# Kernel tuning notes

Measured on AMD Instinct MI355X. Metric: run time of the kernel, lower is better.

## Reference

```python
import jax, jax.numpy as jnp
import numpy as np


def topk_activation(x, k):
    # x: [B, L]; keep top-k per row, zeros elsewhere (torch.topk + scatter_)
    vals, idx = jax.lax.top_k(x, k)            # [B, k]
    rows = jnp.arange(x.shape[0])[:, None]     # [B, 1]
    return jnp.zeros_like(x).at[rows, idx].set(vals)


def setup_inputs() -> dict:
    key = jax.random.key(0)
    k0, k1, k2, k3 = jax.random.split(key, 4)
    B, n_in, n_lat = 4096, 768, 24576
    x = jax.random.normal(k0, (B, n_in), dtype=jnp.float32)
    b = jnp.zeros((n_in,), jnp.float32)
    W_enc = jax.random.normal(k1, (n_lat, n_in), dtype=jnp.float32) * 0.02
    b_enc = jnp.zeros((n_lat,), jnp.float32)
    W_dec = jax.random.normal(k2, (n_in, n_lat), dtype=jnp.float32) * 0.02
    # unit L2 norm per decoder column (as in _normalize_decoder)
    W_dec = W_dec / jnp.clip(jnp.linalg.norm(W_dec, axis=0, keepdims=True), 1e-8)
    miss_counts = jax.random.randint(k3, (n_lat,), 0, 2)  # ~half 'dead' (>=1)
    return {"x": x, "b": b, "W_enc": W_enc, "b_enc": b_enc, "W_dec": W_dec,
            "miss_counts": miss_counts, "k": 32, "aux_k": 512}


def reference(x, b, W_enc, b_enc, W_dec, miss_counts, k, aux_k):
    x_centered = x - b                                   # [B, n_in]
    alpha_pre = x_centered @ W_enc.T + b_enc             # [B, n_lat]
    alpha = topk_activation(alpha_pre, k)                # sparse code
    x_hat = alpha @ W_dec.T + b                          # dense decode
    fired_mask = alpha != 0
    # aux dead-feature path; dead_mask = miss_counts >= threshold(=1).
    # With the chosen miss_counts fill, dead count >> aux_k, so
    # min(aux_k, dead.sum()) == aux_k (static for jit).
    dead_mask = miss_counts >= 1                         # [n_lat]
    alpha_pre_dead = jnp.where(dead_mask[None, :], alpha_pre, -jnp.inf)
    alpha_aux = topk_activation(alpha_pre_dead, aux_k)
    aux_x_hat = alpha_aux @ W_dec.T + b
    return x_hat, alpha, fired_mask, aux_x_hat
```

## Files before the change

kernel.cpp:

```cpp
#include <hip/hip_runtime.h>
#include <math.h>

#define NB   4096
#define NIN  768
#define NLAT 24576
#define K2   1536
#define KT2  24

#define BM 128
#define BN 128
#define BK 16
#define LDT 132

#define CAND_CAP 512
#define BAND_CAP 160
#define MAIN_CAP 64
#define AUX_CAP  1024
#define SELT     1024
#define GRP      6

#define CM_CAP 768
#define CA_CAP 2560
#define BB_CAP 384
#define BPSTRIDE (BAND_CAP + 4)

#define OFF_K16  0
#define OFF_REDF 49152
#define OFF_CTRL 49664
#define OFF_PCNT 49792
#define OFF_CKM  50176
#define OFF_CIM  52224
#define OFF_CKA  54272
#define OFF_CIA  56320
#define OFF_BIM  58368
#define OFF_BIA  59008
#define OFF_BVM  59648
#define OFF_BVA  60928
#define OFF_BSM  62208
#define OFF_BSA  62368
#define OFF_REDI 62528
#define SMEM_SEL 62592

typedef __bf16 bf16x8 __attribute__((ext_vector_type(8)));
typedef float  f32x4  __attribute__((ext_vector_type(4)));

__device__ __forceinline__ unsigned fkey(float f) {
  unsigned u = __float_as_uint(f);
  return u ^ ((unsigned)((int)u >> 31) | 0x80000000u);
}
__device__ __forceinline__ float keyinv(unsigned u) {
  unsigned s = (u & 0x80000000u) ? (u ^ 0x80000000u) : ~u;
  return __uint_as_float(s);
}
__device__ __forceinline__ float zup(float p) {
  p = fminf(fmaxf(p, 1e-7f), 0.5f);
  float t = sqrtf(-2.0f * logf(p));
  return t - (2.30753f + 0.27061f * t) / (1.0f + 0.99229f * t + 0.04481f * t * t);
}

#define GLOAD16(g, l) __builtin_amdgcn_global_load_lds( \
    (const __attribute__((address_space(1))) unsigned int*)(g), \
    (__attribute__((address_space(3))) unsigned int*)(l), 16, 0, 0)

__global__ __launch_bounds__(256) void k_deadbits(const int* __restrict__ miss,
                                                  unsigned* __restrict__ bits) {
  int j = blockIdx.x * 256 + threadIdx.x;
  unsigned long long b = __ballot(miss[j] >= 1);
  if ((threadIdx.x & 63) == 0) {
    int w = j >> 5;
    bits[w] = (unsigned)b;
    bits[w + 1] = (unsigned)(b >> 32);
  }
}

__global__ __launch_bounds__(256) void k_ndead(const unsigned* __restrict__ bits,
                                               int* __restrict__ out) {
  __shared__ int w[4];
  int t = threadIdx.x;
  int c = 0;
  for (int i = t; i < NLAT / 32; i += 256) c += __popc(bits[i]);
#pragma unroll
  for (int o = 32; o; o >>= 1) c += __shfl_xor(c, o);
  if ((t & 63) == 0) w[t >> 6] = c;
  __syncthreads();
  if (t == 0) out[0] = w[0] + w[1] + w[2] + w[3];
}

__global__ __launch_bounds__(256) void k_transpose(const float* __restrict__ src,
                                                   __bf16* __restrict__ dst) {
  __shared__ float tile[32][33];
  int bx = blockIdx.x * 32;
  int by = blockIdx.y * 32;
  int tx = threadIdx.x, ty = threadIdx.y;
  for (int i = ty; i < 32; i += 8)
    tile[i][tx] = src[(size_t)(by + i) * NLAT + bx + tx];
  __syncthreads();
  for (int i = ty; i < 32; i += 8)
    dst[(size_t)(bx + i) * NIN + by + tx] = (__bf16)tile[tx][i];
}

__global__ __launch_bounds__(256) void k_pack_a(const float* __restrict__ x,
    const float* __restrict__ bvec, __bf16* __restrict__ A2) {
  const int mt = blockIdx.x, kt = blockIdx.y, t = threadIdx.x;
  __bf16* out = A2 + (((size_t)mt * KT2 + kt) << 13);
#pragma unroll
  for (int i = 0; i < 32; ++i) {
    int idx = i * 256 + t;
    int r = idx >> 6, c2 = idx & 63;
    int kk = c2 ^ ((r & 7) << 3);
    int kg = kt * 64 + kk;
    int k = kg >= 768 ? kg - 768 : kg;
    bool lo = (kg >= 768);
    float v = x[(size_t)(mt * 128 + r) * NIN + k] - bvec[k];
    __bf16 h = (__bf16)v;
    out[idx] = lo ? (__bf16)(v - (float)h) : h;
  }
}

__global__ __launch_bounds__(256) void k_pack_b(const float* __restrict__ We,
    __bf16* __restrict__ B2) {
  const int nt = blockIdx.x, kt = blockIdx.y, t = threadIdx.x;
  __bf16* out = B2 + (((size_t)nt * KT2 + kt) << 13);
#pragma unroll
  for (int i = 0; i < 32; ++i) {
    int idx = i * 256 + t;
    int r = idx >> 6, c2 = idx & 63;
    int kk = c2 ^ ((r & 7) << 3);
    int kg = kt * 64 + kk;
    int k = kg >= 768 ? kg - 768 : kg;
    float v = We[(size_t)(nt * 128 + r) * NIN + k];
    out[idx] = (__bf16)v;
  }
}

__global__ __launch_bounds__(256) void k_gemm_bf16(
    const __bf16* __restrict__ A2, const __bf16* __restrict__ B2,
    const float* __restrict__ be, float* __restrict__ apre) {
  __shared__ char sA[16384];
  __shared__ char sB[16384];
  const int t = threadIdx.x;
  const int lane = t & 63, wave = t >> 6;
  const int mt = blockIdx.x, nt = blockIdx.y;
  const int wm = wave >> 1, wn = wave & 1;

  int aoff[4][2], boff[4][2];
#pragma unroll
  for (int f = 0; f < 4; ++f) {
    int ra = wm * 64 + f * 16 + (lane & 15);
    int rb = wn * 64 + f * 16 + (lane & 15);
#pragma unroll
    for (int kk = 0; kk < 2; ++kk) {
      int c = kk * 64 + (lane >> 4) * 16;
      aoff[f][kk] = ra * 128 + (c ^ ((ra & 7) << 4));
      boff[f][kk] = rb * 128 + (c ^ ((rb & 7) << 4));
    }
  }
  f32x4 acc[4][4] = {};
  const char* gA = (const char*)(A2 + (((size_t)mt * KT2) << 13));
  const char* gB = (const char*)(B2 + (((size_t)nt * KT2) << 13));
  for (int kt = 0; kt < KT2; ++kt) {
    const char* tA = gA + ((size_t)kt << 14);
    const char* tB = gB + ((size_t)kt << 14);
#pragma unroll
    for (int i = 0; i < 4; ++i) {
      int chunk = (i * 4 + wave) * 1024;
      GLOAD16(tA + chunk + lane * 16, sA + chunk);
      GLOAD16(tB + chunk + lane * 16, sB + chunk);
    }
    __syncthreads();
#pragma unroll
    for (int kk = 0; kk < 2; ++kk) {
      bf16x8 a[4], b[4];
#pragma unroll
      for (int f = 0; f < 4; ++f) {
        a[f] = *(const bf16x8*)(sA + aoff[f][kk]);
        b[f] = *(const bf16x8*)(sB + boff[f][kk]);
      }
#pragma unroll
      for (int mi = 0; mi < 4; ++mi)
#pragma unroll
        for (int ni = 0; ni < 4; ++ni)
          acc[mi][ni] = __builtin_amdgcn_mfma_f32_16x16x32_bf16(a[mi], b[ni], acc[mi][ni], 0, 0, 0);
    }
    __syncthreads();
  }
  const int m0 = mt * 128 + wm * 64, n0 = nt * 128 + wn * 64;
#pragma unroll
  for (int ni = 0; ni < 4; ++ni) {
    int n = n0 + ni * 16 + (lane & 15);
    float bb = be[n];
#pragma unroll
    for (int mi = 0; mi < 4; ++mi) {
      int mbase = m0 + mi * 16 + (lane >> 4) * 4;
#pragma unroll
      for (int q = 0; q < 4; ++q)
        apre[(size_t)(mbase + q) * NLAT + n] = acc[mi][ni][q] + bb;
    }
  }
}

__global__ __launch_bounds__(256) void k_encgemm_f32(
    const float* __restrict__ x, const float* __restrict__ bvec,
    const float* __restrict__ We, const float* __restrict__ be,
    float* __restrict__ apre) {
  __shared__ float As[BK][LDT];
  __shared__ float Bs[BK][LDT];
  const int t = threadIdx.x;
  const int m0 = blockIdx.x * BM;
  const int n0 = blockIdx.y * BN;
  const int lane = t & 63, wave = t >> 6;
  const int cn = ((wave & 1) * 8 + (lane & 7)) * 8;
  const int cm = ((wave >> 1) * 8 + (lane >> 3)) * 8;
  float acc[8][8] = {};
  const float* xb = x + (size_t)m0 * NIN;
  const float* wb = We + (size_t)n0 * NIN;
  for (int k0 = 0; k0 < NIN; k0 += BK) {
#pragma unroll
    for (int i = 0; i < 2; ++i) {
      int e = t + i * 256;
      int row = e >> 2, q = e & 3;
      float4 bv = *(const float4*)(bvec + k0 + q * 4);
      float4 av = *(const float4*)(xb + (size_t)row * NIN + k0 + q * 4);
      av.x -= bv.x; av.y -= bv.y; av.z -= bv.z; av.w -= bv.w;
      As[q * 4 + 0][row] = av.x; As[q * 4 + 1][row] = av.y;
      As[q * 4 + 2][row] = av.z; As[q * 4 + 3][row] = av.w;
      float4 wv = *(const float4*)(wb + (size_t)row * NIN + k0 + q * 4);
      Bs[q * 4 + 0][row] = wv.x; Bs[q * 4 + 1][row] = wv.y;
      Bs[q * 4 + 2][row] = wv.z; Bs[q * 4 + 3][row] = wv.w;
    }
    __syncthreads();
#pragma unroll
    for (int kk = 0; kk < BK; ++kk) {
      float a0[8], b0[8];
      *(float4*)&a0[0] = *(const float4*)&As[kk][cm];
      *(float4*)&a0[4] = *(const float4*)&As[kk][cm + 4];
      *(float4*)&b0[0] = *(const float4*)&Bs[kk][cn];
      *(float4*)&b0[4] = *(const float4*)&Bs[kk][cn + 4];
#pragma unroll
      for (int i = 0; i < 8; ++i)
#pragma unroll
        for (int j = 0; j < 8; ++j)
          acc[i][j] = fmaf(a0[i], b0[j], acc[i][j]);
    }
    __syncthreads();
  }
  float bb[8];
  *(float4*)&bb[0] = *(const float4*)(be + n0 + cn);
  *(float4*)&bb[4] = *(const float4*)(be + n0 + cn + 4);
#pragma unroll
  for (int i = 0; i < 8; ++i) {
    float4 v0 = make_float4(acc[i][0] + bb[0], acc[i][1] + bb[1],
                            acc[i][2] + bb[2], acc[i][3] + bb[3]);
    float4 v1 = make_float4(acc[i][4] + bb[4], acc[i][5] + bb[5],
                            acc[i][6] + bb[6], acc[i][7] + bb[7]);
    float* orow = apre + (size_t)(m0 + cm + i) * NLAT + n0 + cn;
    *(float4*)orow = v0;
    *(float4*)(orow + 4) = v1;
  }
}

__global__ __launch_bounds__(1024) void k_select14(
    const float* __restrict__ apre, const float* __restrict__ x,
    const float* __restrict__ bvec, const float* __restrict__ We,
    const float* __restrict__ be, const unsigned* __restrict__ dbits,
    const int* __restrict__ kptr, const int* __restrict__ akptr,
    const int* __restrict__ ndeadP,
    int* __restrict__ cnts, int* __restrict__ mIdxG, float* __restrict__ mValG,
    int* __restrict__ aIdxG, float* __restrict__ aValG,
    int* __restrict__ bandP, int* __restrict__ flags) {
  __shared__ float redF[32];
  __shared__ float statF[4];
  __shared__ int ctrl[24];
  __shared__ int histM[256];
  __shared__ int histA[256];
  __shared__ uint2 cM[CM_CAP];
  __shared__ uint2 cA[CA_CAP];
  __shared__ uint2 bbM[BB_CAP];
  __shared__ uint2 bbA[BB_CAP];
  __shared__ int biM[BAND_CAP];
  __shared__ int biA[BAND_CAP];
  __shared__ double bvM[BAND_CAP];
  __shared__ double bvA[BAND_CAP];
  __shared__ unsigned char bsM[BAND_CAP];
  __shared__ unsigned char bsA[BAND_CAP];
  unsigned* uctrl = (unsigned*)ctrl;

  const int t = threadIdx.x;
  const int r = blockIdx.x;
  const int lane = t & 63, wave = t >> 6;

  if (t < 24) ctrl[t] = 0;
  if (t >= 256 && t < 512) histM[t - 256] = 0;
  else if (t >= 512 && t < 768) histA[t - 512] = 0;

  const uint4* rowp = (const uint4*)(apre + (size_t)r * NLAT);
  unsigned dm = 0;
  float s1 = 0.f, s2 = 0.f;
#pragma unroll
  for (int i = 0; i < GRP; ++i) {
    int g = t + SELT * i;
    uint4 rv = rowp[g];
    unsigned nb = (dbits[g >> 3] >> ((g & 7) * 4)) & 0xFu;
    dm |= nb << (4 * i);
    float vs[4] = {__uint_as_float(rv.x), __uint_as_float(rv.y),
                   __uint_as_float(rv.z), __uint_as_float(rv.w)};
#pragma unroll
    for (int q = 0; q < 4; ++q) { float v = vs[q]; s1 += v; s2 += v * v; }
  }
#pragma unroll
  for (int o = 32; o; o >>= 1) { s1 += __shfl_xor(s1, o); s2 += __shfl_xor(s2, o); }
  if (lane == 0) { redF[wave] = s1; redF[16 + wave] = s2; }
  __syncthreads();
  if (wave == 0) {
    float a0 = (lane < 16) ? redF[lane] : 0.f;
    float a1 = (lane < 16) ? redF[16 + lane] : 0.f;
#pragma unroll
    for (int o = 32; o; o >>= 1) { a0 += __shfl_xor(a0, o); a1 += __shfl_xor(a1, o); }
    if (lane == 0) {
      float mu = a0 / (float)NLAT;
      float var = fmaxf(a1 / (float)NLAT - mu * mu, 1e-20f);
      statF[0] = mu; statF[1] = sqrtf(var);
    }
  }
  __syncthreads();

  int kmain = kptr[0]; if (kmain > MAIN_CAP) kmain = MAIN_CAP;
  int kaux  = akptr[0]; if (kaux > AUX_CAP)  kaux  = AUX_CAP;
  const int ndead = ndeadP[0];
  int kauxE = kaux > ndead ? ndead : kaux;
  const bool mainOn = (kmain > 0);
  const bool auxOn  = (kauxE > 0);
  const float mu = statF[0], sg = statF[1];
  unsigned TkM = 0xFFFFFFFFu, TkA = 0xFFFFFFFFu;
  if (mainOn) TkM = fkey(mu + sg * zup(8.f * kmain / (float)NLAT));
  if (auxOn) {
    float facA = (3.f * kauxE > 2048.f) ? 2.f : 3.f;
    TkA = fkey(mu + sg * zup(facA * kauxE / (float)ndead));
  }

  unsigned mxM = 0u, mxA = 0u;
#pragma unroll
  for (int i = 0; i < GRP; ++i) {
    int g = t + SELT * i;
    uint4 rv = rowp[g];
    unsigned nb = (dm >> (4 * i)) & 0xFu;
    float vs[4] = {__uint_as_float(rv.x), __uint_as_float(rv.y),
                   __uint_as_float(rv.z), __uint_as_float(rv.w)};
#pragma unroll
    for (int q = 0; q < 4; ++q) {
      unsigned kk = fkey(vs[q]);
      unsigned j = (unsigned)(4 * g + q);
      if (mainOn && kk >= TkM) {
        mxM = kk > mxM ? kk : mxM;
        int p = atomicAdd(&ctrl[0], 1);
        if (p < CM_CAP) { cM[p].x = kk; cM[p].y = j; }
      }
      if (auxOn && ((nb >> q) & 1u) && kk >= TkA) {
        mxA = kk > mxA ? kk : mxA;
        int p = atomicAdd(&ctrl[1], 1);
        if (p < CA_CAP) { cA[p].x = kk; cA[p].y = j; }
      }
    }
  }
#pragma unroll
  for (int o = 32; o; o >>= 1) {
    unsigned a = __shfl_xor(mxM, o); mxM = a > mxM ? a : mxM;
    unsigned b = __shfl_xor(mxA, o); mxA = b > mxA ? b : mxA;
  }
  if (lane == 0) { atomicMax(&uctrl[10], mxM); atomicMax(&uctrl[11], mxA); }
  __syncthreads();
  int ccM = ctrl[0], ccA = ctrl[1];
  bool ok = (!mainOn || (ccM >= kmain && ccM <= CM_CAP)) &&
            (!auxOn  || (ccA >= kauxE && ccA <= CA_CAP));
  if (!ok) { if (t == 0) flags[r] = 1; return; }
  if (!auxOn) ccA = 0;
  if (!mainOn) ccM = 0;
  unsigned MxM = uctrl[10], MxA = uctrl[11];
  float sclM = 255.0f / fmaxf((float)(MxM - TkM) + 1.0f, 1.0f);
  float sclA = 255.0f / fmaxf((float)(MxA - TkA) + 1.0f, 1.0f);

  for (int c = t; c < ccM; c += 1024) {
    int b = (int)((float)(cM[c].x - TkM) * sclM);
    b = b < 0 ? 0 : (b > 255 ? 255 : b);
    atomicAdd(&histM[b], 1);
  }
  for (int c = t; c < ccA; c += 1024) {
    int b = (int)((float)(cA[c].x - TkA) * sclA);
    b = b < 0 ? 0 : (b > 255 ? 255 : b);
    atomicAdd(&histA[b], 1);
  }
  __syncthreads();
  if (t == 0 && mainOn) {
    int above = 0, b = 0;
    for (int i = 255; i >= 0; --i) {
      if (above + histM[i] >= kmain) { b = i; break; }
      above += histM[i];
    }
    ctrl[12] = b; ctrl[13] = above;
  }
  if (t == 64 && auxOn) {
    int above = 0, b = 0;
    for (int i = 255; i >= 0; --i) {
      if (above + histA[i] >= kauxE) { b = i; break; }
      above += histA[i];
    }
    ctrl[14] = b; ctrl[15] = above;
  }
  __syncthreads();
  int bM = ctrl[12], aboveM = ctrl[13];
  int bA = ctrl[14], aboveA = ctrl[15];
  for (int c = t; c < ccM; c += 1024) {
    int b = (int)((float)(cM[c].x - TkM) * sclM);
    b = b < 0 ? 0 : (b > 255 ? 255 : b);
    if (b == bM) {
      int p = atomicAdd(&ctrl[16], 1);
      if (p < BB_CAP) bbM[p] = cM[c];
    }
  }
  for (int c = t; c < ccA; c += 1024) {
    int b = (int)((float)(cA[c].x - TkA) * sclA);
    b = b < 0 ? 0 : (b > 255 ? 255 : b);
    if (b == bA) {
      int p = atomicAdd(&ctrl[17], 1);
      if (p < BB_CAP) bbA[p] = cA[c];
    }
  }
  __syncthreads();
  int nbM = ctrl[16], nbA = ctrl[17];
  if ((mainOn && nbM > BB_CAP) || (auxOn && nbA > BB_CAP)) {
    if (t == 0) flags[r] = 1;
    return;
  }
  if (t == 0) flags[r] = 0;
  if (!mainOn) nbM = 0;
  if (!auxOn) nbA = 0;
  if (t < nbM) {
    uint2 e = bbM[t];
    int rank = 0;
    for (int qq = 0; qq < nbM; ++qq) {
      uint2 f = bbM[qq];
      rank += (f.x > e.x || (f.x == e.x && (int)f.y < (int)e.y)) ? 1 : 0;
    }
    if (rank == kmain - aboveM - 1) ctrl[2] = (int)e.x;
  }
  if (t >= 512 && t - 512 < nbA) {
    uint2 e = bbA[t - 512];
    int rank = 0;
    for (int qq = 0; qq < nbA; ++qq) {
      uint2 f = bbA[qq];
      rank += (f.x > e.x || (f.x == e.x && (int)f.y < (int)e.y)) ? 1 : 0;
    }
    if (rank == kauxE - aboveA - 1) ctrl[3] = (int)e.x;
  }
  __syncthreads();

  float VsM = keyinv((unsigned)ctrl[2]);
  float epsM = 1e-2f + 2e-3f * fabsf(VsM);
  unsigned KhiBM = mainOn ? fkey(VsM + epsM) : 0xFFFFFFFFu;
  unsigned KloBM = mainOn ? fkey(VsM - epsM) : 0xFFFFFFFFu;
  float VsA = keyinv((unsigned)ctrl[3]);
  float epsA = 1e-2f + 2e-3f * fabsf(VsA);
  unsigned KhiBA = auxOn ? fkey(VsA + epsA) : 0xFFFFFFFFu;
  unsigned KloBA = auxOn ? fkey(VsA - epsA) : 0xFFFFFFFFu;
  for (int c = t; c < ccM; c += 1024) {
    unsigned kk = cM[c].x;
    if (kk > KhiBM) atomicAdd(&ctrl[4], 1);
    else if (kk >= KloBM) {
      int p = atomicAdd(&ctrl[5], 1);
      if (p < BAND_CAP) biM[p] = (int)cM[c].y;
    }
  }
  for (int c = t; c < ccA; c += 1024) {
    unsigned kk = cA[c].x;
    if (kk > KhiBA) atomicAdd(&ctrl[6], 1);
    else if (kk >= KloBA) {
      int p = atomicAdd(&ctrl[7], 1);
      if (p < BAND_CAP) biA[p] = (int)cA[c].y;
    }
  }
  __syncthreads();
  int nAbM = ctrl[4], bcM = ctrl[5] < BAND_CAP ? ctrl[5] : BAND_CAP;
  int nAbA = ctrl[6], bcA = ctrl[7] < BAND_CAP ? ctrl[7] : BAND_CAP;
  if (!mainOn) bcM = 0;
  if (!auxOn) bcA = 0;
  int needBM = kmain - nAbM; if (needBM < 0) needBM = 0; if (needBM > bcM) needBM = bcM;
  int needBA = kauxE - nAbA; if (needBA < 0) needBA = 0; if (needBA > bcA) needBA = bcA;

  {
    const float* xr = x + (size_t)r * NIN;
    float xb[NIN / 64];
#pragma unroll
    for (int jj = 0; jj < NIN / 64; ++jj) {
      int col = lane + 64 * jj;
      xb[jj] = xr[col] - bvec[col];
    }
    int tot = bcM + bcA;
    for (int m = wave; m < tot; m += 16) {
      int j = (m < bcM) ? biM[m] : biA[m - bcM];
      const float* wr = We + (size_t)j * NIN;
      double s = 0.0;
#pragma unroll
      for (int jj = 0; jj < NIN / 64; ++jj)
        s += (double)xb[jj] * (double)wr[lane + 64 * jj];
#pragma unroll
      for (int o = 32; o; o >>= 1) s += __shfl_xor(s, o);
      if (lane == 0) {
        if (m < bcM) bvM[m] = s + (double)be[j];
        else bvA[m - bcM] = s + (double)be[j];
      }
    }
  }
  __syncthreads();
  if (t < bcM) {
    double vi = bvM[t]; int ii = biM[t];
    double tie = fabs(vi) * 4e-8 + 1e-12;
    int rank = 0;
    for (int qq = 0; qq < bcM; ++qq) {
      double d = bvM[qq] - vi;
      rank += ((fabs(d) <= tie) ? (biM[qq] < ii) : (d > 0.0)) ? 1 : 0;
    }
    bsM[t] = (rank < needBM) ? 1 : 0;
  }
  if (t >= 512 && t - 512 < bcA) {
    int tt = t - 512;
    double vi = bvA[tt]; int ii = biA[tt];
    double tie = fabs(vi) * 4e-8 + 1e-12;
    int rank = 0;
    for (int qq = 0; qq < bcA; ++qq) {
      double d = bvA[qq] - vi;
      rank += ((fabs(d) <= tie) ? (biA[qq] < ii) : (d > 0.0)) ? 1 : 0;
    }
    bsA[tt] = (rank < needBA) ? 1 : 0;
  }
  __syncthreads();

  for (int c = t; c < ccM; c += 1024) {
    unsigned kk = cM[c].x; int j = (int)cM[c].y;
    bool sel = kk > KhiBM;
    if (!sel && kk >= KloBM) {
      for (int m2 = 0; m2 < bcM; ++m2)
        if (biM[m2] == j) { sel = bsM[m2] != 0; break; }
    }
    float v = keyinv(kk);
    if (sel && v != 0.0f) {
      int p = atomicAdd(&ctrl[8], 1);
      if (p < MAIN_CAP) { mIdxG[r * MAIN_CAP + p] = j; mValG[r * MAIN_CAP + p] = v; }
    }
  }
  for (int c = t; c < ccA; c += 1024) {
    unsigned kk = cA[c].x; int j = (int)cA[c].y;
    bool sel = kk > KhiBA;
    if (!sel && kk >= KloBA) {
      for (int m2 = 0; m2 < bcA; ++m2)
        if (biA[m2] == j) { sel = bsA[m2] != 0; break; }
    }
    float v = keyinv(kk);
    if (sel && v != 0.0f) {
      int p = atomicAdd(&ctrl[9], 1);
      if (p < AUX_CAP) { aIdxG[r * AUX_CAP + p] = j; aValG[r * AUX_CAP + p] = v; }
    }
  }
  __syncthreads();
  int* bp = bandP + (size_t)r * BPSTRIDE;
  if (t == 0) {
    cnts[2 * r] = ctrl[8] < MAIN_CAP ? ctrl[8] : MAIN_CAP;
    cnts[2 * r + 1] = auxOn ? (ctrl[9] < AUX_CAP ? ctrl[9] : AUX_CAP) : 0;
    bp[0] = (int)KhiBM; bp[1] = (int)KloBM; bp[2] = bcM;
  }
  if (t < bcM) bp[3 + t] = (biM[t] << 1) | (int)bsM[t];
}

__global__ __launch_bounds__(256) void k_emit(
    const float* apre, const int* __restrict__ flags,
    const int* __restrict__ bandP, float* __restrict__ alpha, float* mask) {
  const int bid = blockIdx.x;
  const int r = bid / 3, c = bid % 3;
  if (flags[r]) return;
  __shared__ int hdr[3];
  __shared__ int bent[BAND_CAP];
  const int t = threadIdx.x;
  const int* bp = bandP + (size_t)r * BPSTRIDE;
  if (t < 3) hdr[t] = bp[t];
  __syncthreads();
  int bc = hdr[2];
  if (t < bc) bent[t] = bp[3 + t];
  __syncthreads();
  unsigned KhiB = (unsigned)hdr[0], KloB = (unsigned)hdr[1];
  const float4* src = (const float4*)(apre + (size_t)r * NLAT) + c * 2048;
  float4* adst = (float4*)(alpha + (size_t)r * NLAT) + c * 2048;
  float4* mdst = (float4*)(mask + (size_t)r * NLAT) + c * 2048;
  const int ebase = c * 8192;
#pragma unroll
  for (int i = 0; i < 8; ++i) {
    int g = t + 256 * i;
    float4 v4 = src[g];
    float vs[4] = {v4.x, v4.y, v4.z, v4.w};
    float av[4], mv[4];
#pragma unroll
    for (int q = 0; q < 4; ++q) {
      float v = vs[q];
      unsigned kk = fkey(v);
      int j = ebase + 4 * g + q;
      bool sel = kk > KhiB;
      if (!sel && kk >= KloB) {
        for (int m = 0; m < bc; ++m)
          if ((bent[m] >> 1) == j) { sel = (bent[m] & 1) != 0; break; }
      }
      av[q] = sel ? v : 0.0f;
      mv[q] = (sel && v != 0.0f) ? 1.0f : 0.0f;
    }
    adst[g] = make_float4(av[0], av[1], av[2], av[3]);
    mdst[g] = make_float4(mv[0], mv[1], mv[2], mv[3]);
  }
}

__global__ __launch_bounds__(SELT) void k_selectFB(
    const float* apre, const float* __restrict__ x,
    const float* __restrict__ bvec, const float* __restrict__ We,
    const float* __restrict__ be, const unsigned* __restrict__ dbits,
    const int* __restrict__ kptr, const int* __restrict__ akptr,
    float* __restrict__ alpha, float* mask,
    int* __restrict__ cnts, int* __restrict__ mIdxG, float* __restrict__ mValG,
    int* __restrict__ aIdxG, float* __restrict__ aValG,
    const int* __restrict__ flags) {
  if (flags[blockIdx.x] == 0) return;
  extern __shared__ char smem[];
  uint2*    keys2 = (uint2*)(smem + OFF_K16);
  float*    redF  = (float*)(smem + OFF_REDF);
  int*      redI  = (int*)(smem + OFF_REDI);
  int*      ctrl  = (int*)(smem + OFF_CTRL);
  float*    ctrlF = (float*)(smem + OFF_CTRL);
  int*      pcnt  = (int*)(smem + OFF_PCNT);
  unsigned* ckM   = (unsigned*)(smem + OFF_CKM);
  int*      ciM   = (int*)(smem + OFF_CIM);
  unsigned* ckA   = (unsigned*)(smem + OFF_CKA);
  int*      ciA   = (int*)(smem + OFF_CIA);
  int*      biM   = (int*)(smem + OFF_BIM);
  int*      biA   = (int*)(smem + OFF_BIA);
  double*   bvM   = (double*)(smem + OFF_BVM);
  double*   bvA   = (double*)(smem + OFF_BVA);
  unsigned char* bsM = (unsigned char*)(smem + OFF_BSM);
  unsigned char* bsA = (unsigned char*)(smem + OFF_BSA);

  const int t = threadIdx.x;
  const int r = blockIdx.x;
  const int lane = t & 63, wave = t >> 6;

  if (t < 96) pcnt[t] = 0;
  else if (t < 108) ctrl[t - 96] = 0;

  const uint4* rowp = (const uint4*)(apre + (size_t)r * NLAT);
  const float* rowf = apre + (size_t)r * NLAT;
  unsigned dm = 0;
  float s1 = 0.f, s2 = 0.f;
  float vmxA = -INFINITY, vmnA = INFINITY, vmxD = -INFINITY, vmnD = INFINITY;
#pragma unroll
  for (int i = 0; i < GRP; ++i) {
    int g = t + SELT * i;
    uint4 rv = rowp[g];
    unsigned nb = (dbits[g >> 3] >> ((g & 7) * 4)) & 0xFu;
    dm |= nb << (4 * i);
    float vs[4] = {__uint_as_float(rv.x), __uint_as_float(rv.y),
                   __uint_as_float(rv.z), __uint_as_float(rv.w)};
    unsigned k16[4];
#pragma unroll
    for (int q = 0; q < 4; ++q) {
      float v = vs[q];
      k16[q] = fkey(v) >> 16;
      s1 += v; s2 += v * v;
      vmxA = fmaxf(vmxA, v); vmnA = fminf(vmnA, v);
      if ((nb >> q) & 1u) { vmxD = fmaxf(vmxD, v); vmnD = fminf(vmnD, v); }
    }
    uint2 kp2;
    kp2.x = k16[0] | (k16[1] << 16);
    kp2.y = k16[2] | (k16[3] << 16);
    keys2[g] = kp2;
  }
  int nd = __popc(dm & 0xFFFFFFu);
#pragma unroll
  for (int o = 32; o; o >>= 1) {
    s1 += __shfl_xor(s1, o); s2 += __shfl_xor(s2, o);
    vmxA = fmaxf(vmxA, __shfl_xor(vmxA, o)); vmnA = fminf(vmnA, __shfl_xor(vmnA, o));
    vmxD = fmaxf(vmxD, __shfl_xor(vmxD, o)); vmnD = fminf(vmnD, __shfl_xor(vmnD, o));
    nd += __shfl_xor(nd, o);
  }
  if (lane == 0) {
    float* rf = redF + wave * 8;
    rf[0] = s1; rf[1] = s2; rf[2] = vmxA; rf[3] = vmnA; rf[4] = vmxD; rf[5] = vmnD;
    redI[wave] = nd;
  }
  __syncthreads();
  if (wave == 0) {
    float a0 = 0.f, a1 = 0.f, a2 = -INFINITY, a3 = INFINITY, a4 = -INFINITY, a5 = INFINITY;
    int a6 = 0;
    if (lane < 16) {
      const float* rf = redF + lane * 8;
      a0 = rf[0]; a1 = rf[1]; a2 = rf[2]; a3 = rf[3]; a4 = rf[4]; a5 = rf[5];
      a6 = redI[lane];
    }
#pragma unroll
    for (int o = 32; o; o >>= 1) {
      a0 += __shfl_xor(a0, o); a1 += __shfl_xor(a1, o);
      a2 = fmaxf(a2, __shfl_xor(a2, o)); a3 = fminf(a3, __shfl_xor(a3, o));
      a4 = fmaxf(a4, __shfl_xor(a4, o)); a5 = fminf(a5, __shfl_xor(a5, o));
      a6 += __shfl_xor(a6, o);
    }
    if (lane == 0) {
      float mu = a0 / (float)NLAT;
      float var = fmaxf(a1 / (float)NLAT - mu * mu, 1e-20f);
      ctrlF[16] = mu; ctrlF[17] = sqrtf(var);
      ctrlF[18] = a3; ctrlF[19] = a2;
      ctrlF[20] = a5; ctrlF[21] = a4;
      ctrl[22] = a6;
    }
  }
  __syncthreads();

  int kmain = kptr[0]; if (kmain > MAIN_CAP) kmain = MAIN_CAP;
  int kaux  = akptr[0]; if (kaux > AUX_CAP)  kaux  = AUX_CAP;
  const float mu = ctrlF[16], sg = ctrlF[17];
  const int ndead = ctrl[22];
  int kauxE = kaux > ndead ? ndead : kaux;
  const bool mainOn = (kmain > 0);
  const bool auxOn  = (kauxE > 0);

  unsigned TloM = fkey(ctrlF[18]) >> 16, ThiM = (fkey(ctrlF[19]) >> 16) + 1u;
  int cLoM = NLAT, cHiM = 0;
  unsigned TloA = 0u, ThiA = 2u;
  int cLoA = 0, cHiA = 0;
  if (auxOn) { TloA = fkey(ctrlF[20]) >> 16; ThiA = (fkey(ctrlF[21]) >> 16) + 1u; cLoA = ndead; }

  for (int it = 0; it < 16; ++it) {
    bool actM = mainOn && (cLoM - cHiM) > (CAND_CAP - 8) && (ThiM - TloM) > 1u;
    bool actA = auxOn  && (cLoA - cHiA) > (CAND_CAP - 8) && (ThiA - TloA) > 1u;
    if (!actM && !actA) break;
    unsigned TM1 = TloM + 1u, TM2 = TM1, TM3 = TM1;
    unsigned TA1 = TloA + 1u, TA2 = TA1, TA3 = TA1;
    if (actM) {
      unsigned lo1 = TloM + 1u, hi1 = ThiM - 1u;
      if (it == 0) {
        float fn = (float)NLAT;
        TM1 = fkey(mu + sg * zup(4.f * kmain / fn)) >> 16;
        TM2 = fkey(mu + sg * zup((float)kmain / fn)) >> 16;
        TM3 = fkey(mu + sg * zup(0.25f * kmain / fn)) >> 16;
      } else {
        float vlo = keyinv(TloM << 16), vhi = keyinv((ThiM << 16) - 1u);
        TM1 = fkey(0.75f * vlo + 0.25f * vhi) >> 16;
        TM2 = fkey(0.50f * vlo + 0.50f * vhi) >> 16;
        TM3 = fkey(0.25f * vlo + 0.75f * vhi) >> 16;
      }
      TM1 = TM1 < lo1 ? lo1 : (TM1 > hi1 ? hi1 : TM1);
      TM2 = TM2 < TM1 ? TM1 : (TM2 > hi1 ? hi1 : TM2);
      TM3 = TM3 < TM2 ? TM2 : (TM3 > hi1 ? hi1 : TM3);
    }
    if (actA) {
      unsigned lo1 = TloA + 1u, hi1 = ThiA - 1u;
      if (it == 0) {
        float fn = (float)ndead;
        TA1 = fkey(mu + sg * zup(4.f * kauxE / fn)) >> 16;
        TA2 = fkey(mu + sg * zup((float)kauxE / fn)) >> 16;
        TA3 = fkey(mu + sg * zup(0.25f * kauxE / fn)) >> 16;
      } else {
        float vlo = keyinv(TloA << 16), vhi = keyinv((ThiA << 16) - 1u);
        TA1 = fkey(0.75f * vlo + 0.25f * vhi) >> 16;
        TA2 = fkey(0.50f * vlo + 0.50f * vhi) >> 16;
        TA3 = fkey(0.25f * vlo + 0.75f * vhi) >> 16;
      }
      TA1 = TA1 < lo1 ? lo1 : (TA1 > hi1 ? hi1 : TA1);
      TA2 = TA2 < TA1 ? TA1 : (TA2 > hi1 ? hi1 : TA2);
      TA3 = TA3 < TA2 ? TA2 : (TA3 > hi1 ? hi1 : TA3);
    }
    int cm1 = 0, cm2 = 0, cm3 = 0, ca1 = 0, ca2 = 0, ca3 = 0;
#pragma unroll
    for (int i = 0; i < GRP; ++i) {
      uint2 kv = keys2[t + SELT * i];
      unsigned nb = (dm >> (4 * i)) & 0xFu;
      unsigned ks[4] = {kv.x & 0xFFFFu, kv.x >> 16, kv.y & 0xFFFFu, kv.y >> 16};
#pragma unroll
      for (int q = 0; q < 4; ++q) {
        unsigned kk = ks[q];
        cm1 += (kk >= TM1); cm2 += (kk >= TM2); cm3 += (kk >= TM3);
        if ((nb >> q) & 1u) { ca1 += (kk >= TA1); ca2 += (kk >= TA2); ca3 += (kk >= TA3); }
      }
    }
#pragma unroll
    for (int o = 32; o; o >>= 1) {
      cm1 += __shfl_xor(cm1, o); cm2 += __shfl_xor(cm2, o); cm3 += __shfl_xor(cm3, o);
      ca1 += __shfl_xor(ca1, o); ca2 += __shfl_xor(ca2, o); ca3 += __shfl_xor(ca3, o);
    }
    if (lane == 0) {
      int* pc = pcnt + it * 6;
      atomicAdd(&pc[0], cm1); atomicAdd(&pc[1], cm2); atomicAdd(&pc[2], cm3);
      atomicAdd(&pc[3], ca1); atomicAdd(&pc[4], ca2); atomicAdd(&pc[5], ca3);
    }
    __syncthreads();
    const int* pc = pcnt + it * 6;
    int CM1 = pc[0], CM2 = pc[1], CM3 = pc[2];
    int CA1 = pc[3], CA2 = pc[4], CA3 = pc[5];
    if (actM) {
      if (CM3 >= kmain)      { TloM = TM3; cLoM = CM3; }
      else if (CM2 >= kmain) { TloM = TM2; cLoM = CM2; ThiM = TM3; cHiM = CM3; }
      else if (CM1 >= kmain) { TloM = TM1; cLoM = CM1; ThiM = TM2; cHiM = CM2; }
      else                   { ThiM = TM1; cHiM = CM1; }
    }
    if (actA) {
      if (CA3 >= kauxE)      { TloA = TA3; cLoA = CA3; }
      else if (CA2 >= kauxE) { TloA = TA2; cLoA = CA2; ThiA = TA3; cHiA = CA3; }
      else if (CA1 >= kauxE) { TloA = TA1; cLoA = CA1; ThiA = TA2; cHiA = CA2; }
      else                   { ThiA = TA1; cHiA = CA1; }
    }
  }

#pragma unroll
  for (int i = 0; i < GRP; ++i) {
    int g = t + SELT * i;
    uint2 kv = keys2[g];
    unsigned nb = (dm >> (4 * i)) & 0xFu;
    unsigned ks[4] = {kv.x & 0xFFFFu, kv.x >> 16, kv.y & 0xFFFFu, kv.y >> 16};
#pragma unroll
    for (int q = 0; q < 4; ++q) {
      unsigned kk = ks[q];
      int j = 4 * g + q;
      if (mainOn && kk >= TloM && kk < ThiM) {
        int p = atomicAdd(&ctrl[0], 1);
        if (p < CAND_CAP) { ckM[p] = fkey(rowf[j]); ciM[p] = j; }
      }
      if (auxOn && ((nb >> q) & 1u) && kk >= TloA && kk < ThiA) {
        int p = atomicAdd(&ctrl[1], 1);
        if (p < CAND_CAP) { ckA[p] = fkey(rowf[j]); ciA[p] = j; }
      }
    }
  }
  __syncthreads();
  int ccM = ctrl[0] < CAND_CAP ? ctrl[0] : CAND_CAP;
  int ccA = ctrl[1] < CAND_CAP ? ctrl[1] : CAND_CAP;
  int needM = kmain - cHiM; if (needM < 1) needM = 1; if (needM > ccM) needM = ccM;
  int needA = kauxE - cHiA; if (needA < 1) needA = 1; if (needA > ccA) needA = ccA;

  if (t < ccM) {
    unsigned ki = ckM[t]; int ii = ciM[t];
    int rank = 0;
    for (int qq = 0; qq < ccM; ++qq) {
      unsigned kq = ckM[qq];
      rank += (kq > ki || (kq == ki && ciM[qq] < ii)) ? 1 : 0;
    }
    if (rank == needM - 1) ctrl[2] = (int)ki;
  } else if (t >= 512 && t - 512 < ccA) {
    int tt = t - 512;
    unsigned ki = ckA[tt]; int ii = ciA[tt];
    int rank = 0;
    for (int qq = 0; qq < ccA; ++qq) {
      unsigned kq = ckA[qq];
      rank += (kq > ki || (kq == ki && ciA[qq] < ii)) ? 1 : 0;
    }
    if (rank == needA - 1) ctrl[3] = (int)ki;
  }
  __syncthreads();

  float VsM = keyinv((unsigned)ctrl[2]);
  float epsM = 1e-2f + 2e-3f * fabsf(VsM);
  unsigned KhiBM = mainOn ? fkey(VsM + epsM) : 0xFFFFFFFFu;
  unsigned KloBM = mainOn ? fkey(VsM - epsM) : 0xFFFFFFFFu;
  float VsA = keyinv((unsigned)ctrl[3]);
  float epsA = 1e-2f + 2e-3f * fabsf(VsA);
  unsigned KhiBA = auxOn ? fkey(VsA + epsA) : 0xFFFFFFFFu;
  unsigned KloBA = auxOn ? fkey(VsA - epsA) : 0xFFFFFFFFu;
  unsigned KhiBM16 = KhiBM >> 16, KloBM16 = KloBM >> 16;
  unsigned KhiBA16 = KhiBA >> 16, KloBA16 = KloBA >> 16;
  int abvM = 0, abvA = 0;
#pragma unroll
  for (int i = 0; i < GRP; ++i) {
    int g = t + SELT * i;
    uint2 kv = keys2[g];
    unsigned nb = (dm >> (4 * i)) & 0xFu;
    unsigned ks[4] = {kv.x & 0xFFFFu, kv.x >> 16, kv.y & 0xFFFFu, kv.y >> 16};
#pragma unroll
    for (int q = 0; q < 4; ++q) {
      unsigned kk = ks[q];
      int j = 4 * g + q;
      if (mainOn) {
        if (kk > KhiBM16) ++abvM;
        else if (kk >= KloBM16) {
          unsigned kf = fkey(rowf[j]);
          if (kf > KhiBM) ++abvM;
          else if (kf >= KloBM) {
            int p = atomicAdd(&ctrl[5], 1);
            if (p < BAND_CAP) biM[p] = j;
          }
        }
      }
      if (auxOn && ((nb >> q) & 1u)) {
        if (kk > KhiBA16) ++abvA;
        else if (kk >= KloBA16) {
          unsigned kf = fkey(rowf[j]);
          if (kf > KhiBA) ++abvA;
          else if (kf >= KloBA) {
            int p = atomicAdd(&ctrl[7], 1);
            if (p < BAND_CAP) biA[p] = j;
          }
        }
      }
    }
  }
#pragma unroll
  for (int o = 32; o; o >>= 1) { abvM += __shfl_xor(abvM, o); abvA += __shfl_xor(abvA, o); }
  if (lane == 0) { atomicAdd(&ctrl[4], abvM); atomicAdd(&ctrl[6], abvA); }
  __syncthreads();
  int nAbM = ctrl[4], bcM = ctrl[5] < BAND_CAP ? ctrl[5] : BAND_CAP;
  int nAbA = ctrl[6], bcA = auxOn ? (ctrl[7] < BAND_CAP ? ctrl[7] : BAND_CAP) : 0;
  if (!mainOn) bcM = 0;
  int needBM = kmain - nAbM; if (needBM < 0) needBM = 0; if (needBM > bcM) needBM = bcM;
  int needBA = kauxE - nAbA; if (needBA < 0) needBA = 0; if (needBA > bcA) needBA = bcA;

  {
    const float* xr = x + (size_t)r * NIN;
    float xb[NIN / 64];
#pragma unroll
    for (int jj = 0; jj < NIN / 64; ++jj) {
      int col = lane + 64 * jj;
      xb[jj] = xr[col] - bvec[col];
    }
    int tot = bcM + bcA;
    for (int m = wave; m < tot; m += 16) {
      int j = (m < bcM) ? biM[m] : biA[m - bcM];
      const float* wr = We + (size_t)j * NIN;
      double s = 0.0;
#pragma unroll
      for (int jj = 0; jj < NIN / 64; ++jj)
        s += (double)xb[jj] * (double)wr[lane + 64 * jj];
#pragma unroll
      for (int o = 32; o; o >>= 1) s += __shfl_xor(s, o);
      if (lane == 0) {
        if (m < bcM) bvM[m] = s + (double)be[j];
        else bvA[m - bcM] = s + (double)be[j];
      }
    }
  }
  __syncthreads();
  if (t < bcM) {
    double vi = bvM[t]; int ii = biM[t];
    double tie = fabs(vi) * 4e-8 + 1e-12;
    int rank = 0;
    for (int qq = 0; qq < bcM; ++qq) {
      double d = bvM[qq] - vi;
      rank += ((fabs(d) <= tie) ? (biM[qq] < ii) : (d > 0.0)) ? 1 : 0;
    }
    bsM[t] = (rank < needBM) ? 1 : 0;
  } else if (t >= 512 && t - 512 < bcA) {
    int tt = t - 512;
    double vi = bvA[tt]; int ii = biA[tt];
    double tie = fabs(vi) * 4e-8 + 1e-12;
    int rank = 0;
    for (int qq = 0; qq < bcA; ++qq) {
      double d = bvA[qq] - vi;
      rank += ((fabs(d) <= tie) ? (biA[qq] < ii) : (d > 0.0)) ? 1 : 0;
    }
    bsA[tt] = (rank < needBA) ? 1 : 0;
  }
  __syncthreads();

  {
    float4* arow = (float4*)(alpha + (size_t)r * NLAT);
    float4* mrow = (float4*)(mask + (size_t)r * NLAT);
#pragma unroll
    for (int i = 0; i < GRP; ++i) {
      int g = t + SELT * i;
      uint4 rv = rowp[g];
      unsigned nb = (dm >> (4 * i)) & 0xFu;
      float vs[4] = {__uint_as_float(rv.x), __uint_as_float(rv.y),
                     __uint_as_float(rv.z), __uint_as_float(rv.w)};
      float av[4], mv[4];
#pragma unroll
      for (int q = 0; q < 4; ++q) {
        float v = vs[q];
        unsigned kk = fkey(v);
        int j = 4 * g + q;
        bool selM = mainOn && (kk > KhiBM);
        if (mainOn && !selM && kk >= KloBM) {
          for (int m2 = 0; m2 < bcM; ++m2)
            if (biM[m2] == j) { selM = bsM[m2] != 0; break; }
        }
        bool nz = selM && (v != 0.0f);
        av[q] = selM ? v : 0.0f;
        mv[q] = nz ? 1.0f : 0.0f;
        if (nz) {
          int p = atomicAdd(&ctrl[8], 1);
          if (p < MAIN_CAP) { mIdxG[r * MAIN_CAP + p] = j; mValG[r * MAIN_CAP + p] = v; }
        }
        if (auxOn && ((nb >> q) & 1u)) {
          bool selA = kk > KhiBA;
          if (!selA && kk >= KloBA) {
            for (int m2 = 0; m2 < bcA; ++m2)
              if (biA[m2] == j) { selA = bsA[m2] != 0; break; }
          }
          if (selA && v != 0.0f) {
            int p = atomicAdd(&ctrl[9], 1);
            if (p < AUX_CAP) { aIdxG[r * AUX_CAP + p] = j; aValG[r * AUX_CAP + p] = v; }
          }
        }
      }
      arow[g] = make_float4(av[0], av[1], av[2], av[3]);
      mrow[g] = make_float4(mv[0], mv[1], mv[2], mv[3]);
    }
  }
  __syncthreads();
  if (t == 0) {
    cnts[2 * r] = ctrl[8] < MAIN_CAP ? ctrl[8] : MAIN_CAP;
    cnts[2 * r + 1] = auxOn ? (ctrl[9] < AUX_CAP ? ctrl[9] : AUX_CAP) : 0;
  }
}

__global__ __launch_bounds__(256) void k_decode(
    const int* __restrict__ cnts, const int* __restrict__ mIdxG,
    const float* __restrict__ mValG, const int* __restrict__ aIdxG,
    const float* __restrict__ aValG, const float* __restrict__ bvec,
    const __bf16* __restrict__ Wt, const float* __restrict__ Wd,
    float* __restrict__ xhat, float* __restrict__ auxo) {
  const int r = blockIdx.x, t = threadIdx.x;
  __shared__ int sMi[MAIN_CAP];
  __shared__ float sMv[MAIN_CAP];
  __shared__ int sAi[AUX_CAP];
  __shared__ float sAv[AUX_CAP];
  int kc = cnts[2 * r], ac = cnts[2 * r + 1];
  if (t < MAIN_CAP && t < kc) { sMi[t] = mIdxG[r * MAIN_CAP + t]; sMv[t] = mValG[r * MAIN_CAP + t]; }
  for (int i = t; i < ac; i += 256) { sAi[i] = aIdxG[r * AUX_CAP + i]; sAv[i] = aValG[r * AUX_CAP + i]; }
  __syncthreads();

  float o0 = 0.f, o1 = 0.f, o2 = 0.f;
  float a0 = 0.f, a1 = 0.f, a2 = 0.f;
  if (Wt) {
    int i = 0;
    for (; i + 4 <= kc; i += 4) {
      int i0 = sMi[i], i1 = sMi[i + 1], i2 = sMi[i + 2], i3 = sMi[i + 3];
      float v0 = sMv[i], v1 = sMv[i + 1], v2 = sMv[i + 2], v3 = sMv[i + 3];
      const __bf16* p0 = Wt + (size_t)i0 * NIN;
      const __bf16* p1 = Wt + (size_t)i1 * NIN;
      const __bf16* p2 = Wt + (size_t)i2 * NIN;
      const __bf16* p3 = Wt + (size_t)i3 * NIN;
      float w00 = p0[t], w01 = p0[t + 256], w02 = p0[t + 512];
      float w10 = p1[t], w11 = p1[t + 256], w12 = p1[t + 512];
      float w20 = p2[t], w21 = p2[t + 256], w22 = p2[t + 512];
      float w30 = p3[t], w31 = p3[t + 256], w32 = p3[t + 512];
      o0 = fmaf(v0, w00, o0); o1 = fmaf(v0, w01, o1); o2 = fmaf(v0, w02, o2);
      o0 = fmaf(v1, w10, o0); o1 = fmaf(v1, w11, o1); o2 = fmaf(v1, w12, o2);
      o0 = fmaf(v2, w20, o0); o1 = fmaf(v2, w21, o1); o2 = fmaf(v2, w22, o2);
      o0 = fmaf(v3, w30, o0); o1 = fmaf(v3, w31, o1); o2 = fmaf(v3, w32, o2);
    }
    for (; i < kc; ++i) {
      const __bf16* p = Wt + (size_t)sMi[i] * NIN;
      float v = sMv[i];
      o0 = fmaf(v, (float)p[t], o0);
      o1 = fmaf(v, (float)p[t + 256], o1);
      o2 = fmaf(v, (float)p[t + 512], o2);
    }
    i = 0;
    for (; i + 4 <= ac; i += 4) {
      int i0 = sAi[i], i1 = sAi[i + 1], i2 = sAi[i + 2], i3 = sAi[i + 3];
      float v0 = sAv[i], v1 = sAv[i + 1], v2 = sAv[i + 2], v3 = sAv[i + 3];
      const __bf16* p0 = Wt + (size_t)i0 * NIN;
      const __bf16* p1 = Wt + (size_t)i1 * NIN;
      const __bf16* p2 = Wt + (size_t)i2 * NIN;
      const __bf16* p3 = Wt + (size_t)i3 * NIN;
      float w00 = p0[t], w01 = p0[t + 256], w02 = p0[t + 512];
      float w10 = p1[t], w11 = p1[t + 256], w12 = p1[t + 512];
      float w20 = p2[t], w21 = p2[t + 256], w22 = p2[t + 512];
      float w30 = p3[t], w31 = p3[t + 256], w32 = p3[t + 512];
      a0 = fmaf(v0, w00, a0); a1 = fmaf(v0, w01, a1); a2 = fmaf(v0, w02, a2);
      a0 = fmaf(v1, w10, a0); a1 = fmaf(v1, w11, a1); a2 = fmaf(v1, w12, a2);
      a0 = fmaf(v2, w20, a0); a1 = fmaf(v2, w21, a1); a2 = fmaf(v2, w22, a2);
      a0 = fmaf(v3, w30, a0); a1 = fmaf(v3, w31, a1); a2 = fmaf(v3, w32, a2);
    }
    for (; i < ac; ++i) {
      const __bf16* p = Wt + (size_t)sAi[i] * NIN;
      float v = sAv[i];
      a0 = fmaf(v, (float)p[t], a0);
      a1 = fmaf(v, (float)p[t + 256], a1);
      a2 = fmaf(v, (float)p[t + 512], a2);
    }
  } else {
    for (int i = 0; i < kc; ++i) {
      float v = sMv[i]; int ix = sMi[i];
      o0 = fmaf(v, Wd[(size_t)t * NLAT + ix], o0);
      o1 = fmaf(v, Wd[(size_t)(t + 256) * NLAT + ix], o1);
      o2 = fmaf(v, Wd[(size_t)(t + 512) * NLAT + ix], o2);
    }
    for (int i = 0; i < ac; ++i) {
      float v = sAv[i]; int ix = sAi[i];
      a0 = fmaf(v, Wd[(size_t)t * NLAT + ix], a0);
      a1 = fmaf(v, Wd[(size_t)(t + 256) * NLAT + ix], a1);
      a2 = fmaf(v, Wd[(size_t)(t + 512) * NLAT + ix], a2);
    }
  }
  float b0 = bvec[t], b1 = bvec[t + 256], b2 = bvec[t + 512];
  xhat[(size_t)r * NIN + t] = o0 + b0;
  xhat[(size_t)r * NIN + t + 256] = o1 + b1;
  xhat[(size_t)r * NIN + t + 512] = o2 + b2;
  auxo[(size_t)r * NIN + t] = a0 + b0;
  auxo[(size_t)r * NIN + t + 256] = a1 + b1;
  auxo[(size_t)r * NIN + t + 512] = a2 + b2;
}

extern "C" void kernel_launch(void* const* d_in, const int* in_sizes, int n_in,
                              void* d_out, int out_size, void* d_ws, size_t ws_size,
                              hipStream_t stream) {
  const float* x  = (const float*)d_in[0];
  const float* bv = (const float*)d_in[1];
  const float* We = (const float*)d_in[2];
  const float* be = (const float*)d_in[3];
  const float* Wd = (const float*)d_in[4];
  const int* miss = (const int*)d_in[5];
  const int* kp   = (const int*)d_in[6];
  const int* akp  = (const int*)d_in[7];

  float* out   = (float*)d_out;
  float* xhat  = out;
  float* alpha = out + (size_t)3145728;
  float* apre  = out + (size_t)103809024;
  float* auxo  = out + (size_t)204472320;

  char* wsb = (char*)d_ws;
  size_t o = 0;
  unsigned* dbits = (unsigned*)(wsb + o); o += 65536;
  int*   cnts  = (int*)(wsb + o); o += 65536;
  int*   mIdxG = (int*)(wsb + o); o += (size_t)NB * MAIN_CAP * 4;
  float* mValG = (float*)(wsb + o); o += (size_t)NB * MAIN_CAP * 4;
  int*   aIdxG = (int*)(wsb + o); o += (size_t)NB * AUX_CAP * 4;
  float* aValG = (float*)(wsb + o); o += (size_t)NB * AUX_CAP * 4;
  int*   bandP = (int*)(wsb + o); o += (size_t)NB * BPSTRIDE * 4;
  int*   flags = (int*)(wsb + o); o += 65536;
  int*   ndead = (int*)(wsb + o); o += 65536;
  size_t offWt = o;
  size_t offA2 = offWt + (size_t)NLAT * NIN * 2;
  size_t offB2 = offA2 + (size_t)NB * K2 * 2;
  size_t needFull = offB2 + (size_t)NLAT * K2 * 2;
  bool haveWt   = ws_size >= offA2;
  bool haveFull = ws_size >= needFull;
  __bf16* Wt = haveWt ? (__bf16*)(wsb + offWt) : nullptr;
  __bf16* A2 = (__bf16*)(wsb + offA2);
  __bf16* B2 = (__bf16*)(wsb + offB2);

  k_deadbits<<<96, 256, 0, stream>>>(miss, dbits);
  k_ndead<<<1, 256, 0, stream>>>(dbits, ndead);
  if (haveFull) {
    k_pack_a<<<dim3(32, KT2), 256, 0, stream>>>(x, bv, A2);
    k_pack_b<<<dim3(192, KT2), 256, 0, stream>>>(We, B2);
  }
  if (haveWt)
    k_transpose<<<dim3(NLAT / 32, NIN / 32), dim3(32, 8), 0, stream>>>(Wd, Wt);

  if (haveFull)
    k_gemm_bf16<<<dim3(32, 192), 256, 0, stream>>>(A2, B2, be, apre);
  else
    k_encgemm_f32<<<dim3(NB / BM, NLAT / BN), 256, 0, stream>>>(x, bv, We, be, apre);

  k_select14<<<NB, 1024, 0, stream>>>(apre, x, bv, We, be, dbits, kp, akp, ndead,
                                      cnts, mIdxG, mValG, aIdxG, aValG, bandP, flags);
  k_selectFB<<<NB, SELT, SMEM_SEL, stream>>>(apre, x, bv, We, be, dbits, kp, akp,
                                             alpha, apre, cnts, mIdxG, mValG,
                                             aIdxG, aValG, flags);
  k_emit<<<NB * 3, 256, 0, stream>>>(apre, flags, bandP, alpha, apre);
  k_decode<<<NB, 256, 0, stream>>>(cnts, mIdxG, mValG, aIdxG, aValG, bv,
                                   Wt, Wd, xhat, auxo);
}
```

Before: 1.545 ms.

## Fuse emit pass into select kernel and swizzle GEMM tile order

```diff
diff --git a/kernel.cpp b/kernel.cpp
--- a/kernel.cpp
+++ b/kernel.cpp
@@ -22,7 +22,6 @@
 #define CM_CAP 768
 #define CA_CAP 2560
 #define BB_CAP 384
-#define BPSTRIDE (BAND_CAP + 4)
 
 #define OFF_K16  0
 #define OFF_REDF 49152
@@ -140,7 +139,9 @@
   __shared__ char sB[16384];
   const int t = threadIdx.x;
   const int lane = t & 63, wave = t >> 6;
-  const int mt = blockIdx.x, nt = blockIdx.y;
+  int flat = blockIdx.y * 32 + blockIdx.x;
+  int nf = (flat & 7) * 768 + (flat >> 3);
+  const int mt = nf & 31, nt = nf >> 5;
   const int wm = wave >> 1, wn = wave & 1;
 
   int aoff[4][2], boff[4][2];
@@ -259,15 +260,16 @@
   }
 }
 
-__global__ __launch_bounds__(1024) void k_select14(
-    const float* __restrict__ apre, const float* __restrict__ x,
+__global__ __launch_bounds__(1024) void k_select15(
+    const float* apre, const float* __restrict__ x,
     const float* __restrict__ bvec, const float* __restrict__ We,
     const float* __restrict__ be, const unsigned* __restrict__ dbits,
     const int* __restrict__ kptr, const int* __restrict__ akptr,
     const int* __restrict__ ndeadP,
+    float* __restrict__ alpha, float* mask,
     int* __restrict__ cnts, int* __restrict__ mIdxG, float* __restrict__ mValG,
     int* __restrict__ aIdxG, float* __restrict__ aValG,
-    int* __restrict__ bandP, int* __restrict__ flags) {
+    int* __restrict__ flags) {
   __shared__ float redF[32];
   __shared__ float statF[4];
   __shared__ int ctrl[24];
@@ -561,56 +563,37 @@
     }
   }
   __syncthreads();
-  int* bp = bandP + (size_t)r * BPSTRIDE;
   if (t == 0) {
     cnts[2 * r] = ctrl[8] < MAIN_CAP ? ctrl[8] : MAIN_CAP;
     cnts[2 * r + 1] = auxOn ? (ctrl[9] < AUX_CAP ? ctrl[9] : AUX_CAP) : 0;
-    bp[0] = (int)KhiBM; bp[1] = (int)KloBM; bp[2] = bcM;
-  }
-  if (t < bcM) bp[3 + t] = (biM[t] << 1) | (int)bsM[t];
-}
-
-__global__ __launch_bounds__(256) void k_emit(
-    const float* apre, const int* __restrict__ flags,
-    const int* __restrict__ bandP, float* __restrict__ alpha, float* mask) {
-  const int bid = blockIdx.x;
-  const int r = bid / 3, c = bid % 3;
-  if (flags[r]) return;
-  __shared__ int hdr[3];
-  __shared__ int bent[BAND_CAP];
-  const int t = threadIdx.x;
-  const int* bp = bandP + (size_t)r * BPSTRIDE;
-  if (t < 3) hdr[t] = bp[t];
-  __syncthreads();
-  int bc = hdr[2];
-  if (t < bc) bent[t] = bp[3 + t];
-  __syncthreads();
-  unsigned KhiB = (unsigned)hdr[0], KloB = (unsigned)hdr[1];
-  const float4* src = (const float4*)(apre + (size_t)r * NLAT) + c * 2048;
-  float4* adst = (float4*)(alpha + (size_t)r * NLAT) + c * 2048;
-  float4* mdst = (float4*)(mask + (size_t)r * NLAT) + c * 2048;
-  const int ebase = c * 8192;
-#pragma unroll
-  for (int i = 0; i < 8; ++i) {
-    int g = t + 256 * i;
-    float4 v4 = src[g];
-    float vs[4] = {v4.x, v4.y, v4.z, v4.w};
-    float av[4], mv[4];
-#pragma unroll
-    for (int q = 0; q < 4; ++q) {
-      float v = vs[q];
-      unsigned kk = fkey(v);
-      int j = ebase + 4 * g + q;
-      bool sel = kk > KhiB;
-      if (!sel && kk >= KloB) {
-        for (int m = 0; m < bc; ++m)
-          if ((bent[m] >> 1) == j) { sel = (bent[m] & 1) != 0; break; }
-      }
-      av[q] = sel ? v : 0.0f;
-      mv[q] = (sel && v != 0.0f) ? 1.0f : 0.0f;
-    }
-    adst[g] = make_float4(av[0], av[1], av[2], av[3]);
-    mdst[g] = make_float4(mv[0], mv[1], mv[2], mv[3]);
+  }
+
+  {
+    float4* arow = (float4*)(alpha + (size_t)r * NLAT);
+    float4* mrow = (float4*)(mask + (size_t)r * NLAT);
+#pragma unroll
+    for (int i = 0; i < GRP; ++i) {
+      int g = t + SELT * i;
+      uint4 rv = rowp[g];
+      float vs[4] = {__uint_as_float(rv.x), __uint_as_float(rv.y),
+                     __uint_as_float(rv.z), __uint_as_float(rv.w)};
+      float av[4], mv[4];
+#pragma unroll
+      for (int q = 0; q < 4; ++q) {
+        float v = vs[q];
+        unsigned kk = fkey(v);
+        int j = 4 * g + q;
+        bool sel = kk > KhiBM;
+        if (!sel && kk >= KloBM) {
+          for (int m2 = 0; m2 < bcM; ++m2)
+            if (biM[m2] == j) { sel = bsM[m2] != 0; break; }
+        }
+        av[q] = sel ? v : 0.0f;
+        mv[q] = (sel && v != 0.0f) ? 1.0f : 0.0f;
+      }
+      arow[g] = make_float4(av[0], av[1], av[2], av[3]);
+      mrow[g] = make_float4(mv[0], mv[1], mv[2], mv[3]);
+    }
   }
 }
 
@@ -1126,7 +1109,6 @@
   float* mValG = (float*)(wsb + o); o += (size_t)NB * MAIN_CAP * 4;
   int*   aIdxG = (int*)(wsb + o); o += (size_t)NB * AUX_CAP * 4;
   float* aValG = (float*)(wsb + o); o += (size_t)NB * AUX_CAP * 4;
-  int*   bandP = (int*)(wsb + o); o += (size_t)NB * BPSTRIDE * 4;
   int*   flags = (int*)(wsb + o); o += 65536;
   int*   ndead = (int*)(wsb + o); o += 65536;
   size_t offWt = o;
@@ -1153,12 +1135,12 @@
   else
     k_encgemm_f32<<<dim3(NB / BM, NLAT / BN), 256, 0, stream>>>(x, bv, We, be, apre);
 
-  k_select14<<<NB, 1024, 0, stream>>>(apre, x, bv, We, be, dbits, kp, akp, ndead,
-                                      cnts, mIdxG, mValG, aIdxG, aValG, bandP, flags);
+  k_select15<<<NB, 1024, 0, stream>>>(apre, x, bv, We, be, dbits, kp, akp, ndead,
+                                      alpha, apre, cnts, mIdxG, mValG, aIdxG,
+                                      aValG, flags);
   k_selectFB<<<NB, SELT, SMEM_SEL, stream>>>(apre, x, bv, We, be, dbits, kp, akp,
                                              alpha, apre, cnts, mIdxG, mValG,
                                              aIdxG, aValG, flags);
-  k_emit<<<NB * 3, 256, 0, stream>>>(apre, flags, bandP, alpha, apre);
   k_decode<<<NB, 256, 0, stream>>>(cnts, mIdxG, mValG, aIdxG, aValG, bv,
                                    Wt, Wd, xhat, auxo);
 }
```

Result: slower. 1.680 ms (+8.7%).
